# Kernel tuning notes

Measured on AMD Instinct MI355X. Metric: run time of the kernel, lower is better.

Reference implementation:

```python
import jax, jax.numpy as jnp
import numpy as np

NUM_TNETS = 8388608
NUM_PINS = 20971520
NUM_NODES = 1048576

def setup_inputs() -> dict:
    key = jax.random.key(0)
    k1, k2, k3 = jax.random.split(key, 3)
    beta = jax.random.uniform(k1, (1,), dtype=jnp.float32)
    tnet_weights = jax.random.uniform(k2, (NUM_TNETS,), dtype=jnp.float32)
    flat_tnet2pin = jax.random.randint(k3, (2 * NUM_TNETS,), 0, NUM_PINS, dtype=jnp.int64)
    pin2node_map = jax.random.randint(jax.random.fold_in(key, 7), (NUM_PINS,), 0, NUM_NODES, dtype=jnp.int64)
    return {
        "beta": beta,
        "tnet_weights": tnet_weights,
        "flat_tnet2pin": flat_tnet2pin,
        "pin2node_map": pin2node_map,
    }

def reference(beta, tnet_weights, flat_tnet2pin, pin2node_map):
    # flat_tnet2pin layout: [src_0, dst_0, src_1, dst_1, ...] (2 pins per timing arc)
    # gather node id for every arc pin: [2*num_tnets]
    node_idx = pin2node_map[flat_tnet2pin]
    # each arc's weight is added at both its source and sink node
    w = jnp.repeat(tnet_weights, 2)  # [w0, w0, w1, w1, ...] matches flat layout
    out = jnp.zeros(NUM_NODES, dtype=jnp.float32).at[node_idx].add(w)
    return out * beta
```

## Files before the change

### kernel.cpp

```cpp
#include <hip/hip_runtime.h>
#include <stdint.h>


#define TILE 4096
#define THREADS 512
#define IPT  8
#define NB1  40
#define SHIFT1 19
#define CAP1 430080
#define TPB1 105
#define NB2  64
#define SHIFT2 14
#define CAP2 270336
#define ACC_NODES 16384
#define PARTS 8
#define CHK (CAP2 / PARTS)
#define CTRL_BYTES 8192

typedef unsigned long long item_t;
typedef int   int4_ev   __attribute__((ext_vector_type(4)));
typedef float float4_ev __attribute__((ext_vector_type(4)));
typedef unsigned long long ull2_ev __attribute__((ext_vector_type(2)));

__device__ __forceinline__ item_t pack_item(uint32_t key, float w) {
    return (item_t)key | ((item_t)__float_as_uint(w) << 32);
}

__device__ __forceinline__ void multisplit_flush(
    uint32_t (&key)[IPT], float (&wv)[IPT], int (&bin)[IPT],
    int tile_cnt, int shift,
    int* __restrict__ gcur, item_t* __restrict__ gout, size_t cap)
{
    __shared__ int hist[256];
    __shared__ int basex[256];
    __shared__ int gbase[256];
    __shared__ int wsum[4];
    __shared__ item_t stage[TILE];
    const int t = threadIdx.x;

    if (t < 256) hist[t] = 0;
    __syncthreads();

    int rank[IPT];
#pragma unroll
    for (int k = 0; k < IPT; ++k)
        rank[k] = (bin[k] >= 0) ? atomicAdd(&hist[bin[k]], 1) : 0;
    __syncthreads();

    int val = (t < 256) ? hist[t] : 0;
    int inc = val;
#pragma unroll
    for (int d = 1; d < 64; d <<= 1) {
        int n = __shfl_up(inc, d, 64);
        if ((t & 63) >= d) inc += n;
    }
    if (t < 256 && (t & 63) == 63) wsum[t >> 6] = inc;
    __syncthreads();
    if (t < 256) {
        int w = t >> 6, prefix = 0;
        if (w > 0) prefix += wsum[0];
        if (w > 1) prefix += wsum[1];
        if (w > 2) prefix += wsum[2];
        basex[t] = prefix + inc - val;
        gbase[t] = (val > 0) ? atomicAdd(&gcur[t], val) : 0;
    }
    __syncthreads();

#pragma unroll
    for (int k = 0; k < IPT; ++k) {
        if (bin[k] >= 0)
            stage[basex[bin[k]] + rank[k]] = pack_item(key[k], wv[k]);
    }
    __syncthreads();

    for (int j = t; j < tile_cnt; j += THREADS) {
        item_t e = stage[j];
        int b = (int)((uint32_t)(e & 0xffffffffull) >> shift);
        long long dst = (long long)gbase[b] + (j - basex[b]);
        if (dst >= 0 && dst < (long long)cap)
            __builtin_nontemporal_store(e, &gout[(size_t)b * cap + (size_t)dst]);
    }
}

__global__ __launch_bounds__(THREADS, 8) void k1_partition_pins(
    const int* __restrict__ flat_pins, const float* __restrict__ weights,
    int* __restrict__ cur1, item_t* __restrict__ items1, int total)
{
    const int tileBase = blockIdx.x * TILE;
    const int t = threadIdx.x;
    const int base = tileBase + t * IPT;
    uint32_t key[IPT]; float wv[IPT]; int bin[IPT];

    if (base + IPT <= total) {
        int4_ev   p[2];
        float4_ev w;
#pragma unroll
        for (int v = 0; v < 2; ++v)
            p[v] = __builtin_nontemporal_load((const int4_ev*)(flat_pins + base) + v);
        w = __builtin_nontemporal_load((const float4_ev*)(weights + (base >> 1)));
#pragma unroll
        for (int k = 0; k < IPT; ++k) {
            int pin = p[k >> 2][k & 3];
            key[k] = (uint32_t)pin;
            wv[k]  = w[(k >> 1) & 3];
            bin[k] = pin >> SHIFT1;
        }
    } else {
#pragma unroll
        for (int k = 0; k < IPT; ++k) {
            int i = base + k;
            bool ok = i < total;
            int pin = ok ? flat_pins[i] : 0;
            key[k] = (uint32_t)pin;
            wv[k]  = ok ? weights[i >> 1] : 0.f;
            bin[k] = ok ? (pin >> SHIFT1) : -1;
        }
    }
    int cnt = min(TILE, total - tileBase);
    multisplit_flush(key, wv, bin, cnt, SHIFT1, cur1, items1, (size_t)CAP1);
}

__global__ __launch_bounds__(THREADS, 8) void k2_gather_partition(
    const item_t* __restrict__ items1, const int* __restrict__ cur1,
    const int* __restrict__ pin2node,
    int* __restrict__ cur2, item_t* __restrict__ items2)
{
    const int q = blockIdx.x;
    const int r = q & 7;
    const int s = q >> 3;
    const int bin  = r + 8 * (s / TPB1);
    const int tile = s % TPB1;
    const int cnt = min(cur1[bin], (int)CAP1);
    const int tbase = tile * TILE;
    if (tbase >= cnt) return;

    const item_t* src = items1 + (size_t)bin * CAP1;
    const int t = threadIdx.x;
    const int base = tbase + t * IPT;
    uint32_t key[IPT]; float wv[IPT]; int b2[IPT];

    if (base + IPT <= cnt) {
        ull2_ev it[4];
#pragma unroll
        for (int v = 0; v < 4; ++v)
            it[v] = __builtin_nontemporal_load((const ull2_ev*)(src + base) + v);
#pragma unroll
        for (int k = 0; k < IPT; ++k) {
            item_t e = it[k >> 1][k & 1];
            int node = pin2node[(uint32_t)(e & 0xffffffffull)];
            key[k] = (uint32_t)node;
            wv[k]  = __uint_as_float((uint32_t)(e >> 32));
            b2[k]  = node >> SHIFT2;
        }
    } else {
#pragma unroll
        for (int k = 0; k < IPT; ++k) {
            int i = base + k;
            bool ok = i < cnt;
            item_t e = ok ? src[i] : 0ull;
            int node = ok ? pin2node[(uint32_t)(e & 0xffffffffull)] : 0;
            key[k] = (uint32_t)node;
            wv[k]  = __uint_as_float((uint32_t)(e >> 32));
            b2[k]  = ok ? (node >> SHIFT2) : -1;
        }
    }
    int tcnt = min(TILE, cnt - tbase);
    multisplit_flush(key, wv, b2, tcnt, SHIFT2, cur2, items2, (size_t)CAP2);
}

__global__ __launch_bounds__(1024, 8) void k3_accumulate_part(
    const item_t* __restrict__ items2, const int* __restrict__ cur2,
    float* __restrict__ partials)
{
    __shared__ float acc[ACC_NODES];
    const int b = blockIdx.x >> 3;
    const int p = blockIdx.x & (PARTS - 1);
    const int t = threadIdx.x;
    for (int i = t; i < ACC_NODES; i += 1024) acc[i] = 0.f;
    __syncthreads();

    const int cnt = min(cur2[b], (int)CAP2);
    const int lo  = p * CHK;
    const int hi  = min(cnt, lo + CHK);
    const item_t* src = items2 + (size_t)b * CAP2;

    const int nv = (hi > lo) ? ((hi - lo) >> 2) : 0;
    for (int g = t; g < nv; g += 1024) {
        const item_t* pp = src + lo + ((size_t)g << 2);
        ull2_ev a0 = __builtin_nontemporal_load((const ull2_ev*)pp);
        ull2_ev a1 = __builtin_nontemporal_load((const ull2_ev*)pp + 1);
#pragma unroll
        for (int k = 0; k < 2; ++k) {
            item_t e0 = a0[k], e1 = a1[k];
            atomicAdd(&acc[(uint32_t)(e0 & 0xffffffffull) & (ACC_NODES - 1)],
                      __uint_as_float((uint32_t)(e0 >> 32)));
            atomicAdd(&acc[(uint32_t)(e1 & 0xffffffffull) & (ACC_NODES - 1)],
                      __uint_as_float((uint32_t)(e1 >> 32)));
        }
    }
    for (int i = lo + (nv << 2) + t; i < hi; i += 1024) {
        item_t e = __builtin_nontemporal_load(&src[i]);
        atomicAdd(&acc[(uint32_t)(e & 0xffffffffull) & (ACC_NODES - 1)],
                  __uint_as_float((uint32_t)(e >> 32)));
    }
    __syncthreads();

    float* __restrict__ dst = partials + (size_t)blockIdx.x * ACC_NODES;
    for (int i = t; i < ACC_NODES; i += 1024) dst[i] = acc[i];
}

__global__ __launch_bounds__(256) void k4_reduce(
    const float* __restrict__ partials, const float* __restrict__ beta,
    float* __restrict__ out, int num_nodes)
{
    const float bt = beta[0];
    const int n = (blockIdx.x * 256 + threadIdx.x) << 2;
    if (n + 3 < num_nodes) {
        const int b   = n >> SHIFT2;
        const int off = n & (ACC_NODES - 1);
        const float* base = partials + ((size_t)b * PARTS) * ACC_NODES + off;
        float4_ev s = {0.f, 0.f, 0.f, 0.f};
#pragma unroll
        for (int p = 0; p < PARTS; ++p)
            s += *(const float4_ev*)(base + (size_t)p * ACC_NODES);
        *(float4_ev*)(out + n) = s * bt;
    } else {
        for (int k = 0; k < 4; ++k) {
            int nn = n + k;
            if (nn < num_nodes) {
                const int b   = nn >> SHIFT2;
                const int off = nn & (ACC_NODES - 1);
                float s = 0.f;
#pragma unroll
                for (int p = 0; p < PARTS; ++p)
                    s += partials[((size_t)b * PARTS + p) * ACC_NODES + off];
                out[nn] = s * bt;
            }
        }
    }
}

__global__ __launch_bounds__(256) void scatter_device(
    const float* __restrict__ beta, const float* __restrict__ tnet_weights,
    const long long* __restrict__ pin_pairs, const int* __restrict__ pin2node_map,
    float* __restrict__ out, int num_tnets)
{
    int t = blockIdx.x * blockDim.x + threadIdx.x;
    if (t >= num_tnets) return;
    long long pp = pin_pairs[t];
    float w = tnet_weights[t] * beta[0];
    atomicAdd(&out[pin2node_map[(int)(pp & 0xffffffffLL)]], w);
    atomicAdd(&out[pin2node_map[(int)(pp >> 32)]], w);
}

extern "C" void kernel_launch(void* const* d_in, const int* in_sizes, int n_in,
                              void* d_out, int out_size, void* d_ws, size_t ws_size,
                              hipStream_t stream) {
    const float* beta         = (const float*)d_in[0];
    const float* weights      = (const float*)d_in[1];
    const int*   flat_pins    = (const int*)d_in[2];
    const int*   pin2node     = (const int*)d_in[3];
    float* out = (float*)d_out;

    const int num_tnets = in_sizes[1];
    const int total     = in_sizes[2];
    const int num_nodes = out_size;

    const size_t items1Bytes = (size_t)NB1 * CAP1 * sizeof(item_t);
    const size_t items2Bytes = (size_t)NB2 * CAP2 * sizeof(item_t);
    const size_t partBytes   = (size_t)NB2 * PARTS * ACC_NODES * sizeof(float);

    int* cur1 = (int*)d_ws;
    int* cur2 = (int*)((char*)d_ws + 2048);
    const int gridTiles = (total + TILE - 1) / TILE;

    if (ws_size >= CTRL_BYTES + items1Bytes + items2Bytes + partBytes) {
        item_t* items1 = (item_t*)((char*)d_ws + CTRL_BYTES);
        item_t* items2 = (item_t*)((char*)d_ws + CTRL_BYTES + items1Bytes);
        float*  partials = (float*)((char*)d_ws + CTRL_BYTES + items1Bytes + items2Bytes);
        (void)hipMemsetAsync(d_ws, 0, CTRL_BYTES, stream);
        k1_partition_pins<<<gridTiles, THREADS, 0, stream>>>(
            flat_pins, weights, cur1, items1, total);
        k2_gather_partition<<<NB1 * TPB1, THREADS, 0, stream>>>(
            items1, cur1, pin2node, cur2, items2);
        k3_accumulate_part<<<NB2 * PARTS, 1024, 0, stream>>>(
            items2, cur2, partials);
        const int i4slots = (num_nodes + 3) / 4;
        k4_reduce<<<(i4slots + 255) / 256, 256, 0, stream>>>(
            partials, beta, out, num_nodes);
    } else {
        (void)hipMemsetAsync(d_out, 0, (size_t)out_size * sizeof(float), stream);
        scatter_device<<<(num_tnets + 255) / 256, 256, 0, stream>>>(
            beta, weights, (const long long*)flat_pins, pin2node, out, num_tnets);
    }
}
```

Baseline: 452.3 us.

## Split each bin's global cursor into 8 cache-line-padded sub-cursors per bin

```diff
diff --git a/kernel.cpp b/kernel.cpp
--- a/kernel.cpp
+++ b/kernel.cpp
@@ -7,15 +7,15 @@
 #define IPT  8
 #define NB1  40
 #define SHIFT1 19
-#define CAP1 430080
-#define TPB1 105
+#define CAP1R 55296
+#define TPB1R 14
 #define NB2  64
 #define SHIFT2 14
-#define CAP2 270336
+#define CAP2R 34816
 #define ACC_NODES 16384
 #define PARTS 8
-#define CHK (CAP2 / PARTS)
-#define CTRL_BYTES 8192
+#define CLINE_INTS 16
+#define CTRL_BYTES 65536
 
 typedef unsigned long long item_t;
 typedef int   int4_ev   __attribute__((ext_vector_type(4)));
@@ -29,7 +29,8 @@
 __device__ __forceinline__ void multisplit_flush(
     uint32_t (&key)[IPT], float (&wv)[IPT], int (&bin)[IPT],
     int tile_cnt, int shift,
-    int* __restrict__ gcur, item_t* __restrict__ gout, size_t cap)
+    int* __restrict__ gcur, int gcur_stride,
+    item_t* __restrict__ gout, size_t bin_stride, size_t cap)
 {
     __shared__ int hist[256];
     __shared__ int basex[256];
@@ -62,7 +63,7 @@
         if (w > 1) prefix += wsum[1];
         if (w > 2) prefix += wsum[2];
         basex[t] = prefix + inc - val;
-        gbase[t] = (val > 0) ? atomicAdd(&gcur[t], val) : 0;
+        gbase[t] = (val > 0) ? atomicAdd(&gcur[t * gcur_stride], val) : 0;
     }
     __syncthreads();
 
@@ -78,15 +79,16 @@
         int b = (int)((uint32_t)(e & 0xffffffffull) >> shift);
         long long dst = (long long)gbase[b] + (j - basex[b]);
         if (dst >= 0 && dst < (long long)cap)
-            __builtin_nontemporal_store(e, &gout[(size_t)b * cap + (size_t)dst]);
+            __builtin_nontemporal_store(e, &gout[(size_t)b * bin_stride + (size_t)dst]);
     }
 }
 
 __global__ __launch_bounds__(THREADS, 8) void k1_partition_pins(
     const int* __restrict__ flat_pins, const float* __restrict__ weights,
-    int* __restrict__ cur1, item_t* __restrict__ items1, int total)
+    int* __restrict__ ctrl1, item_t* __restrict__ items1, int total)
 {
     const int tileBase = blockIdx.x * TILE;
+    const int r = blockIdx.x & 7;
     const int t = threadIdx.x;
     const int base = tileBase + t * IPT;
     uint32_t key[IPT]; float wv[IPT]; int bin[IPT];
@@ -117,24 +119,30 @@
         }
     }
     int cnt = min(TILE, total - tileBase);
-    multisplit_flush(key, wv, bin, cnt, SHIFT1, cur1, items1, (size_t)CAP1);
+    multisplit_flush(key, wv, bin, cnt, SHIFT1,
+                     ctrl1 + r * CLINE_INTS, 8 * CLINE_INTS,
+                     items1 + (size_t)r * CAP1R, (size_t)8 * CAP1R,
+                     (size_t)CAP1R);
 }
 
 __global__ __launch_bounds__(THREADS, 8) void k2_gather_partition(
-    const item_t* __restrict__ items1, const int* __restrict__ cur1,
+    const item_t* __restrict__ items1, const int* __restrict__ ctrl1,
     const int* __restrict__ pin2node,
-    int* __restrict__ cur2, item_t* __restrict__ items2)
+    int* __restrict__ ctrl2, item_t* __restrict__ items2)
 {
     const int q = blockIdx.x;
-    const int r = q & 7;
-    const int s = q >> 3;
-    const int bin  = r + 8 * (s / TPB1);
-    const int tile = s % TPB1;
-    const int cnt = min(cur1[bin], (int)CAP1);
+    const int r2 = q & 7;
+    const int s  = q >> 3;
+    const int g    = s / (8 * TPB1R);
+    const int rem  = s % (8 * TPB1R);
+    const int r_w  = rem / TPB1R;
+    const int tile = rem % TPB1R;
+    const int bin  = r2 + 8 * g;
+    const int cnt = min(ctrl1[(bin * 8 + r_w) * CLINE_INTS], (int)CAP1R);
     const int tbase = tile * TILE;
     if (tbase >= cnt) return;
 
-    const item_t* src = items1 + (size_t)bin * CAP1;
+    const item_t* src = items1 + ((size_t)bin * 8 + (size_t)r_w) * CAP1R;
     const int t = threadIdx.x;
     const int base = tbase + t * IPT;
     uint32_t key[IPT]; float wv[IPT]; int b2[IPT];
@@ -165,11 +173,14 @@
         }
     }
     int tcnt = min(TILE, cnt - tbase);
-    multisplit_flush(key, wv, b2, tcnt, SHIFT2, cur2, items2, (size_t)CAP2);
+    multisplit_flush(key, wv, b2, tcnt, SHIFT2,
+                     ctrl2 + r2 * CLINE_INTS, 8 * CLINE_INTS,
+                     items2 + (size_t)r2 * CAP2R, (size_t)8 * CAP2R,
+                     (size_t)CAP2R);
 }
 
 __global__ __launch_bounds__(1024, 8) void k3_accumulate_part(
-    const item_t* __restrict__ items2, const int* __restrict__ cur2,
+    const item_t* __restrict__ items2, const int* __restrict__ ctrl2,
     float* __restrict__ partials)
 {
     __shared__ float acc[ACC_NODES];
@@ -179,14 +190,12 @@
     for (int i = t; i < ACC_NODES; i += 1024) acc[i] = 0.f;
     __syncthreads();
 
-    const int cnt = min(cur2[b], (int)CAP2);
-    const int lo  = p * CHK;
-    const int hi  = min(cnt, lo + CHK);
-    const item_t* src = items2 + (size_t)b * CAP2;
-
-    const int nv = (hi > lo) ? ((hi - lo) >> 2) : 0;
+    const int cnt = min(ctrl2[(b * 8 + p) * CLINE_INTS], (int)CAP2R);
+    const item_t* src = items2 + ((size_t)b * 8 + (size_t)p) * CAP2R;
+
+    const int nv = cnt >> 2;
     for (int g = t; g < nv; g += 1024) {
-        const item_t* pp = src + lo + ((size_t)g << 2);
+        const item_t* pp = src + ((size_t)g << 2);
         ull2_ev a0 = __builtin_nontemporal_load((const ull2_ev*)pp);
         ull2_ev a1 = __builtin_nontemporal_load((const ull2_ev*)pp + 1);
 #pragma unroll
@@ -198,7 +207,7 @@
                       __uint_as_float((uint32_t)(e1 >> 32)));
         }
     }
-    for (int i = lo + (nv << 2) + t; i < hi; i += 1024) {
+    for (int i = (nv << 2) + t; i < cnt; i += 1024) {
         item_t e = __builtin_nontemporal_load(&src[i]);
         atomicAdd(&acc[(uint32_t)(e & 0xffffffffull) & (ACC_NODES - 1)],
                   __uint_as_float((uint32_t)(e >> 32)));
@@ -266,12 +275,12 @@
     const int total     = in_sizes[2];
     const int num_nodes = out_size;
 
-    const size_t items1Bytes = (size_t)NB1 * CAP1 * sizeof(item_t);
-    const size_t items2Bytes = (size_t)NB2 * CAP2 * sizeof(item_t);
+    const size_t items1Bytes = (size_t)NB1 * 8 * CAP1R * sizeof(item_t);
+    const size_t items2Bytes = (size_t)NB2 * 8 * CAP2R * sizeof(item_t);
     const size_t partBytes   = (size_t)NB2 * PARTS * ACC_NODES * sizeof(float);
 
-    int* cur1 = (int*)d_ws;
-    int* cur2 = (int*)((char*)d_ws + 2048);
+    int* ctrl1 = (int*)d_ws;
+    int* ctrl2 = (int*)((char*)d_ws + 32768);
     const int gridTiles = (total + TILE - 1) / TILE;
 
     if (ws_size >= CTRL_BYTES + items1Bytes + items2Bytes + partBytes) {
@@ -280,11 +289,11 @@
         float*  partials = (float*)((char*)d_ws + CTRL_BYTES + items1Bytes + items2Bytes);
         (void)hipMemsetAsync(d_ws, 0, CTRL_BYTES, stream);
         k1_partition_pins<<<gridTiles, THREADS, 0, stream>>>(
-            flat_pins, weights, cur1, items1, total);
-        k2_gather_partition<<<NB1 * TPB1, THREADS, 0, stream>>>(
-            items1, cur1, pin2node, cur2, items2);
+            flat_pins, weights, ctrl1, items1, total);
+        k2_gather_partition<<<NB1 * 8 * TPB1R, THREADS, 0, stream>>>(
+            items1, ctrl1, pin2node, ctrl2, items2);
         k3_accumulate_part<<<NB2 * PARTS, 1024, 0, stream>>>(
-            items2, cur2, partials);
+            items2, ctrl2, partials);
         const int i4slots = (num_nodes + 3) / 4;
         k4_reduce<<<(i4slots + 255) / 256, 256, 0, stream>>>(
             partials, beta, out, num_nodes);
```

New measurement: 434.4 us. 1.04x faster.
